# Kernel optimization log

Hardware: AMD Instinct MI355X
Metric: run time of the kernel (lower is better)

The kernel has to match this reference:

```python
import jax, jax.numpy as jnp
import numpy as np

C = 4096
IN_DIM = 256
OUT_DIM = 64
H = 4
NEG_SLOPE = 0.2


def setup_inputs() -> dict:
    key = jax.random.key(0)
    k_x, k_adj, k_w, k_as, k_ad = jax.random.split(key, 5)
    x = jax.random.normal(k_x, (C, IN_DIM), dtype=jnp.float32)
    adj = jax.random.randint(k_adj, (C, C), 0, 2, dtype=jnp.int32)
    # xavier_uniform for Linear(in, out*H): bound = sqrt(6/(fan_in+fan_out))
    bw = float(np.sqrt(6.0 / (IN_DIM + OUT_DIM * H)))
    W = jax.random.uniform(k_w, (IN_DIM, OUT_DIM * H), minval=-bw, maxval=bw, dtype=jnp.float32)
    ba = float(np.sqrt(6.0 / (H + OUT_DIM)))
    a_src = jax.random.uniform(k_as, (H, OUT_DIM), minval=-ba, maxval=ba, dtype=jnp.float32)
    a_dst = jax.random.uniform(k_ad, (H, OUT_DIM), minval=-ba, maxval=ba, dtype=jnp.float32)
    return {"x": x, "adj": adj, "W": W, "a_src": a_src, "a_dst": a_dst}


def reference(x, adj, W, a_src, a_dst):
    # h: [C, H, D] -> h_heads: [H, C, D]
    h = (x @ W).reshape(C, H, OUT_DIM)
    h_heads = jnp.transpose(h, (1, 0, 2))
    # per-node additive attention logits: [H, C]
    alpha_src = jnp.einsum('hcd,hd->hc', h_heads, a_src)
    alpha_dst = jnp.einsum('hcd,hd->hc', h_heads, a_dst)
    # broadcast scores e: [H, C, C]
    e = alpha_src[:, :, None] + alpha_dst[:, None, :]
    e = jnp.where(e >= 0, e, NEG_SLOPE * e)  # LeakyReLU
    e = jnp.where(adj[None, :, :] == 0, -jnp.inf, e)
    attn = jax.nn.softmax(e, axis=-1)  # [H, C, C]
    out = jnp.einsum('hcj,hjd->hcd', attn, h_heads)  # [H, C, D]
    return jnp.transpose(out, (1, 0, 2)).reshape(C, H * OUT_DIM)
```

## Files before the change

kernel.cpp:

```cpp
#include <hip/hip_runtime.h>
#include <math.h>

#define CN 4096
#define KDIM 256
#define ND 256
#define NH 4
#define DD 64
#define NEG 0.2f
#define L2E 1.44269504f

typedef __attribute__((ext_vector_type(8))) short short8;
typedef __attribute__((ext_vector_type(4))) float floatx4;

union S8I4 { int i[4]; short8 s; };

__device__ inline unsigned bfbits_rne(float f) {
  unsigned u = __float_as_uint(f);
  u += 0x7fffu + ((u >> 16) & 1u);
  return u >> 16;
}
__device__ inline float bf2f(unsigned hi) { return __uint_as_float(hi << 16); }

__device__ inline int pack2_trunc(float a, float b) {
  return (int)__builtin_amdgcn_perm(__float_as_uint(b), __float_as_uint(a), 0x07060302u);
}

#define GLDS(gp, lp, sz)                                                        \
  __builtin_amdgcn_global_load_lds(                                             \
      (const __attribute__((address_space(1))) void*)(gp),                      \
      (__attribute__((address_space(3))) void*)(lp), (sz), 0, 0)

__global__ __launch_bounds__(256) void k_prep(const int* __restrict__ adj,
                                              unsigned long long* __restrict__ mbits,
                                              const float* __restrict__ W,
                                              unsigned short* __restrict__ WT_hi,
                                              unsigned short* __restrict__ WT_lo) {
  const int bx = blockIdx.x;
  const int t = threadIdx.x;
  if (bx < 4096) {
    const int w = t >> 6, lane = t & 63;
    const size_t base = ((size_t)(bx * 4 + w)) * 1024;
#pragma unroll 4
    for (int it = 0; it < 16; ++it) {
      const size_t idx = base + (size_t)it * 64 + lane;
      const unsigned long long m = __ballot(adj[idx] != 0);
      if (lane == 0) mbits[idx >> 6] = m;
    }
  } else {
    const int c = (bx - 4096) * 4 + (t >> 6);
    const int k0 = (t & 63) * 4;
    unsigned h[4], l[4];
#pragma unroll
    for (int j = 0; j < 4; ++j) {
      const float w = W[(size_t)(k0 + j) * ND + c];
      h[j] = bfbits_rne(w);
      l[j] = bfbits_rne(w - bf2f(h[j]));
    }
    uint2 vh, vl;
    vh.x = h[0] | (h[1] << 16); vh.y = h[2] | (h[3] << 16);
    vl.x = l[0] | (l[1] << 16); vl.y = l[2] | (l[3] << 16);
    *(uint2*)&WT_hi[(size_t)c * KDIM + k0] = vh;
    *(uint2*)&WT_lo[(size_t)c * KDIM + k0] = vl;
  }
}

__global__ __launch_bounds__(256, 2) void k_gemm_h(const float* __restrict__ x,
                                                   const unsigned short* __restrict__ WT_hi,
                                                   const unsigned short* __restrict__ WT_lo,
                                                   const float* __restrict__ a_src,
                                                   const float* __restrict__ a_dst,
                                                   unsigned short* __restrict__ hT,
                                                   float* __restrict__ asrc,
                                                   float* __restrict__ adst) {
  __shared__ __align__(16) unsigned short Whi_s[64 * 264];
  __shared__ __align__(16) unsigned short Wlo_s[64 * 264];
  const int t = threadIdx.x;
  const int lane = t & 63, ww = t >> 6;
  const int n = lane & 15, q = lane >> 4;
  const int head = blockIdx.x;
  const int i0 = blockIdx.y * 64 + ww * 16;
#pragma unroll
  for (int p = 0; p < 8; ++p) {
    const int s = p * 256 + t;
    const int c = s >> 5, kseg = s & 31;
    const size_t g = (size_t)(head * 64 + c) * KDIM + kseg * 8;
    *(short8*)&Whi_s[c * 264 + kseg * 8] = *(const short8*)(WT_hi + g);
    *(short8*)&Wlo_s[c * 264 + kseg * 8] = *(const short8*)(WT_lo + g);
  }
  const float* xr = x + (size_t)(i0 + n) * KDIM + q * 8;
  float4 xa = *(const float4*)(xr);
  float4 xb = *(const float4*)(xr + 4);
  __syncthreads();
  floatx4 acc[4] = {};
  for (int k0 = 0; k0 < KDIM; k0 += 32) {
    const float xs[8] = {xa.x, xa.y, xa.z, xa.w, xb.x, xb.y, xb.z, xb.w};
    if (k0 + 32 < KDIM) {
      xa = *(const float4*)(xr + k0 + 32);
      xb = *(const float4*)(xr + k0 + 36);
    }
    S8I4 Ah, Al;
#pragma unroll
    for (int e = 0; e < 4; ++e) {
      const unsigned h0 = bfbits_rne(xs[2 * e]), h1 = bfbits_rne(xs[2 * e + 1]);
      const float r0 = xs[2 * e] - bf2f(h0), r1 = xs[2 * e + 1] - bf2f(h1);
      Ah.i[e] = (int)(h0 | (h1 << 16));
      Al.i[e] = (int)(bfbits_rne(r0) | (bfbits_rne(r1) << 16));
    }
#pragma unroll
    for (int tt = 0; tt < 4; ++tt) {
      const int boff = (tt * 16 + n) * 264 + k0 + q * 8;
      const short8 Bh = *(const short8*)&Whi_s[boff];
      const short8 Bl = *(const short8*)&Wlo_s[boff];
      acc[tt] = __builtin_amdgcn_mfma_f32_16x16x32_bf16(Ah.s, Bh, acc[tt], 0, 0, 0);
      acc[tt] = __builtin_amdgcn_mfma_f32_16x16x32_bf16(Al.s, Bh, acc[tt], 0, 0, 0);
      acc[tt] = __builtin_amdgcn_mfma_f32_16x16x32_bf16(Ah.s, Bl, acc[tt], 0, 0, 0);
    }
  }
  unsigned short* hTb = hT + (size_t)head * DD * CN;
#pragma unroll
  for (int tt = 0; tt < 4; ++tt)
#pragma unroll
    for (int r = 0; r < 4; r += 2) {
      const unsigned d = bfbits_rne(acc[tt][r]) | (bfbits_rne(acc[tt][r + 1]) << 16);
      *(unsigned*)(hTb + (size_t)(tt * 16 + n) * CN + i0 + q * 4 + r) = d;
    }
  float ps[4] = {}, pd[4] = {};
#pragma unroll
  for (int tt = 0; tt < 4; ++tt) {
    const float as = a_src[head * DD + tt * 16 + n];
    const float ad = a_dst[head * DD + tt * 16 + n];
#pragma unroll
    for (int r = 0; r < 4; ++r) {
      ps[r] += acc[tt][r] * as;
      pd[r] += acc[tt][r] * ad;
    }
  }
#pragma unroll
  for (int off = 1; off < 16; off <<= 1)
#pragma unroll
    for (int r = 0; r < 4; ++r) {
      ps[r] += __shfl_xor(ps[r], off);
      pd[r] += __shfl_xor(pd[r], off);
    }
  if (n == 0) {
#pragma unroll
    for (int r = 0; r < 4; ++r) {
      asrc[head * CN + i0 + q * 4 + r] = ps[r] * L2E;
      adst[head * CN + i0 + q * 4 + r] = pd[r] * L2E;
    }
  }
}

__global__ __launch_bounds__(256, 2) void k_attn(const unsigned short* __restrict__ hT,
                                                 const unsigned* __restrict__ mbits32,
                                                 const float* __restrict__ asrc,
                                                 const float* __restrict__ adst,
                                                 float* __restrict__ out) {
  __shared__ __align__(16) char smem[4 * 2 * 8704];
  const int t = threadIdx.x;
  const int lane = t & 63, ww = t >> 6;
  const int n = lane & 15, q = lane >> 4;
  const int head = blockIdx.y;
  const int i0 = blockIdx.x * 32;
  const unsigned short* __restrict__ hTb = hT + (size_t)head * DD * CN;
  const float* __restrict__ adh = adst + head * CN;
  const int jbase = ww * 1024;

  float sp0 = asrc[head * CN + i0 + n];
  float sp1 = asrc[head * CN + i0 + 16 + n];
  asm volatile("" : "+v"(sp0), "+v"(sp1));

  const int dl = lane >> 3, jbl = (lane & 7) ^ (lane >> 3);
  const unsigned hoff = (unsigned)dl * CN + jbl * 8;
  const unsigned moff = (unsigned)(i0 + (lane >> 1)) * 128 + (lane & 1);
  char* const wbase = smem + ww * 2 * 8704;

  short8 ONES;
#pragma unroll
  for (int u = 0; u < 8; ++u) ONES[u] = (short)0x3F80;

  floatx4 acc[2][4] = {};
  floatx4 accz[2] = {};

  auto ISSUE = [&](int b, int j0) {
    char* base = wbase + b * 8704;
#pragma unroll
    for (int w8 = 0; w8 < 8; ++w8)
      GLDS(hTb + (size_t)(w8 * 8) * CN + hoff + j0, base + w8 * 1024, 16);
    GLDS(mbits32 + moff + (j0 >> 5), base + 8192, 4);
    GLDS(adh + j0 + lane, base + 8448, 4);
  };

  ISSUE(0, jbase);
  for (int c = 0; c < 16; ++c) {
    const int b = c & 1;
    const int jn = jbase + ((c + 1) & 15) * 64;
    ISSUE(b ^ 1, jn);
    asm volatile("s_waitcnt vmcnt(10)" ::: "memory");
    const char* base = wbase + b * 8704;
    short8 B[4][2];
#pragma unroll
    for (int tt = 0; tt < 4; ++tt)
#pragma unroll
      for (int f = 0; f < 2; ++f)
        B[tt][f] = *(const short8*)(base + (tt * 16 + n) * 128 +
                                    ((((f << 2) | q) ^ (n & 7)) << 4));
    const uint2 mk0 = *(const uint2*)(base + 8192 + n * 8);
    const uint2 mk1 = *(const uint2*)(base + 8192 + (16 + n) * 8);
    const float* adl = (const float*)(base + 8448);
#pragma unroll
    for (int f = 0; f < 2; ++f) {
      const float4 a0 = *(const float4*)(adl + f * 32 + q * 8);
      const float4 a1 = *(const float4*)(adl + f * 32 + q * 8 + 4);
      const float ade[8] = {a0.x, a0.y, a0.z, a0.w, a1.x, a1.y, a1.z, a1.w};
#pragma unroll
      for (int rg = 0; rg < 2; ++rg) {
        const unsigned mw = f ? (rg ? mk1.y : mk0.y) : (rg ? mk1.x : mk0.x);
        const unsigned mbyte = (mw >> (q * 8)) & 255u;
        const float sp = rg ? sp1 : sp0;
        float fv[8];
#pragma unroll
        for (int e = 0; e < 8; ++e) {
          float xv = sp + ade[e];
          xv = fmaxf(xv, NEG * xv);
          xv = ((mbyte >> e) & 1u) ? xv : -1e38f;
          fv[e] = __builtin_amdgcn_exp2f(xv);
        }
        S8I4 A;
#pragma unroll
        for (int e = 0; e < 4; ++e) A.i[e] = pack2_trunc(fv[2 * e], fv[2 * e + 1]);
        accz[rg] = __builtin_amdgcn_mfma_f32_16x16x32_bf16(A.s, ONES, accz[rg], 0, 0, 0);
#pragma unroll
        for (int tt = 0; tt < 4; ++tt)
          acc[rg][tt] =
              __builtin_amdgcn_mfma_f32_16x16x32_bf16(A.s, B[tt][f], acc[rg][tt], 0, 0, 0);
      }
    }
  }

  __syncthreads();
  float* red = (float*)smem;
  if (ww > 0) {
#pragma unroll
    for (int rg = 0; rg < 2; ++rg) {
      float* rb = red + ((ww - 1) * 2 + rg) * 1280;
#pragma unroll
      for (int tt = 0; tt < 4; ++tt)
#pragma unroll
        for (int r = 0; r < 4; ++r) rb[(tt * 4 + r) * 64 + lane] = acc[rg][tt][r];
#pragma unroll
      for (int r = 0; r < 4; ++r) rb[(16 + r) * 64 + lane] = accz[rg][r];
    }
  }
  __syncthreads();
  if (ww == 0) {
#pragma unroll
    for (int s = 0; s < 3; ++s)
#pragma unroll
      for (int rg = 0; rg < 2; ++rg) {
        const float* rb = red + (s * 2 + rg) * 1280;
#pragma unroll
        for (int tt = 0; tt < 4; ++tt)
#pragma unroll
          for (int r = 0; r < 4; ++r) acc[rg][tt][r] += rb[(tt * 4 + r) * 64 + lane];
#pragma unroll
        for (int r = 0; r < 4; ++r) accz[rg][r] += rb[(16 + r) * 64 + lane];
      }
#pragma unroll
    for (int rg = 0; rg < 2; ++rg)
#pragma unroll
      for (int r = 0; r < 4; ++r) {
        const float iz = 1.0f / accz[rg][r];
        float* orow = out + (size_t)(i0 + rg * 16 + q * 4 + r) * ND + head * DD + n;
#pragma unroll
        for (int tt = 0; tt < 4; ++tt) orow[tt * 16] = acc[rg][tt][r] * iz;
      }
  }
}

extern "C" void kernel_launch(void* const* d_in, const int* in_sizes, int n_in,
                              void* d_out, int out_size, void* d_ws, size_t ws_size,
                              hipStream_t stream) {
  const float* x = (const float*)d_in[0];
  const int* adj = (const int*)d_in[1];
  const float* W = (const float*)d_in[2];
  const float* a_src = (const float*)d_in[3];
  const float* a_dst = (const float*)d_in[4];
  float* out = (float*)d_out;

  unsigned short* hT = (unsigned short*)d_ws;
  float* asrc = (float*)(hT + (size_t)NH * DD * CN);
  float* adst = asrc + (size_t)NH * CN;
  unsigned short* WT_hi = (unsigned short*)(adst + (size_t)NH * CN);
  unsigned short* WT_lo = WT_hi + (size_t)ND * KDIM;
  unsigned long long* mbits = (unsigned long long*)(WT_lo + (size_t)ND * KDIM);

  k_prep<<<dim3(4096 + ND / 4), 256, 0, stream>>>(adj, mbits, W, WT_hi, WT_lo);
  k_gemm_h<<<dim3(NH, CN / 64), 256, 0, stream>>>(x, WT_hi, WT_lo, a_src, a_dst,
                                                  hT, asrc, adst);
  k_attn<<<dim3(CN / 32, NH), 256, 0, stream>>>(hT, (const unsigned*)mbits,
                                                asrc, adst, out);
}
```

Baseline: 151.9 us.

## Split attention key range across eight waves with smaller per-wave chunks

```diff
diff --git a/kernel.cpp b/kernel.cpp
--- a/kernel.cpp
+++ b/kernel.cpp
@@ -151,12 +151,12 @@
   }
 }
 
-__global__ __launch_bounds__(256, 2) void k_attn(const unsigned short* __restrict__ hT,
+__global__ __launch_bounds__(512, 4) void k_attn(const unsigned short* __restrict__ hT,
                                                  const unsigned* __restrict__ mbits32,
                                                  const float* __restrict__ asrc,
                                                  const float* __restrict__ adst,
                                                  float* __restrict__ out) {
-  __shared__ __align__(16) char smem[4 * 2 * 8704];
+  __shared__ __align__(16) char smem[8 * 2 * 4608];
   const int t = threadIdx.x;
   const int lane = t & 63, ww = t >> 6;
   const int n = lane & 15, q = lane >> 4;
@@ -164,16 +164,16 @@
   const int i0 = blockIdx.x * 32;
   const unsigned short* __restrict__ hTb = hT + (size_t)head * DD * CN;
   const float* __restrict__ adh = adst + head * CN;
-  const int jbase = ww * 1024;
-
-  float sp0 = asrc[head * CN + i0 + n];
-  float sp1 = asrc[head * CN + i0 + 16 + n];
-  asm volatile("" : "+v"(sp0), "+v"(sp1));
-
-  const int dl = lane >> 3, jbl = (lane & 7) ^ (lane >> 3);
-  const unsigned hoff = (unsigned)dl * CN + jbl * 8;
-  const unsigned moff = (unsigned)(i0 + (lane >> 1)) * 128 + (lane & 1);
-  char* const wbase = smem + ww * 2 * 8704;
+  const int jbase = ww * 512;
+
+  const float sp0 = asrc[head * CN + i0 + n];
+  const float sp1 = asrc[head * CN + i0 + 16 + n];
+
+  const unsigned hoff =
+      (unsigned)(lane >> 2) * CN + (((lane & 3) ^ ((lane >> 3) & 3)) * 8);
+  const unsigned mrow = (unsigned)(i0 + (lane & 31)) * 128;
+  const unsigned arow = (unsigned)(lane & 31);
+  char* const wbase = smem + ww * 2 * 4608;
 
   short8 ONES;
 #pragma unroll
@@ -183,89 +183,88 @@
   floatx4 accz[2] = {};
 
   auto ISSUE = [&](int b, int j0) {
-    char* base = wbase + b * 8704;
-#pragma unroll
-    for (int w8 = 0; w8 < 8; ++w8)
-      GLDS(hTb + (size_t)(w8 * 8) * CN + hoff + j0, base + w8 * 1024, 16);
-    GLDS(mbits32 + moff + (j0 >> 5), base + 8192, 4);
-    GLDS(adh + j0 + lane, base + 8448, 4);
+    char* base = wbase + b * 4608;
+#pragma unroll
+    for (int g = 0; g < 4; ++g)
+      GLDS(hTb + (size_t)(g * 16) * CN + hoff + j0, base + g * 1024, 16);
+    GLDS(mbits32 + mrow + (j0 >> 5), base + 4096, 4);
+    GLDS(adh + j0 + arow, base + 4352, 4);
   };
 
   ISSUE(0, jbase);
   for (int c = 0; c < 16; ++c) {
-    const int b = c & 1;
-    const int jn = jbase + ((c + 1) & 15) * 64;
-    ISSUE(b ^ 1, jn);
-    asm volatile("s_waitcnt vmcnt(10)" ::: "memory");
-    const char* base = wbase + b * 8704;
-    short8 B[4][2];
+    if (c < 15) {
+      ISSUE((c + 1) & 1, jbase + (c + 1) * 32);
+      asm volatile("s_waitcnt vmcnt(6)" ::: "memory");
+    } else {
+      asm volatile("s_waitcnt vmcnt(0)" ::: "memory");
+    }
+    const char* base = wbase + (c & 1) * 4608;
+    short8 B[4];
 #pragma unroll
     for (int tt = 0; tt < 4; ++tt)
-#pragma unroll
-      for (int f = 0; f < 2; ++f)
-        B[tt][f] = *(const short8*)(base + (tt * 16 + n) * 128 +
-                                    ((((f << 2) | q) ^ (n & 7)) << 4));
-    const uint2 mk0 = *(const uint2*)(base + 8192 + n * 8);
-    const uint2 mk1 = *(const uint2*)(base + 8192 + (16 + n) * 8);
-    const float* adl = (const float*)(base + 8448);
-#pragma unroll
-    for (int f = 0; f < 2; ++f) {
-      const float4 a0 = *(const float4*)(adl + f * 32 + q * 8);
-      const float4 a1 = *(const float4*)(adl + f * 32 + q * 8 + 4);
-      const float ade[8] = {a0.x, a0.y, a0.z, a0.w, a1.x, a1.y, a1.z, a1.w};
-#pragma unroll
-      for (int rg = 0; rg < 2; ++rg) {
-        const unsigned mw = f ? (rg ? mk1.y : mk0.y) : (rg ? mk1.x : mk0.x);
-        const unsigned mbyte = (mw >> (q * 8)) & 255u;
-        const float sp = rg ? sp1 : sp0;
-        float fv[8];
-#pragma unroll
-        for (int e = 0; e < 8; ++e) {
-          float xv = sp + ade[e];
-          xv = fmaxf(xv, NEG * xv);
-          xv = ((mbyte >> e) & 1u) ? xv : -1e38f;
-          fv[e] = __builtin_amdgcn_exp2f(xv);
-        }
-        S8I4 A;
-#pragma unroll
-        for (int e = 0; e < 4; ++e) A.i[e] = pack2_trunc(fv[2 * e], fv[2 * e + 1]);
-        accz[rg] = __builtin_amdgcn_mfma_f32_16x16x32_bf16(A.s, ONES, accz[rg], 0, 0, 0);
-#pragma unroll
-        for (int tt = 0; tt < 4; ++tt)
-          acc[rg][tt] =
-              __builtin_amdgcn_mfma_f32_16x16x32_bf16(A.s, B[tt][f], acc[rg][tt], 0, 0, 0);
+      B[tt] = *(const short8*)(base + (tt * 16 + n) * 64 +
+                               ((q ^ ((n >> 1) & 3)) << 4));
+    const unsigned m0 = *(const unsigned*)(base + 4096 + n * 4);
+    const unsigned m1 = *(const unsigned*)(base + 4096 + (16 + n) * 4);
+    const float* adl = (const float*)(base + 4352);
+    const float4 a0 = *(const float4*)(adl + q * 8);
+    const float4 a1 = *(const float4*)(adl + q * 8 + 4);
+    const float ade[8] = {a0.x, a0.y, a0.z, a0.w, a1.x, a1.y, a1.z, a1.w};
+#pragma unroll
+    for (int rg = 0; rg < 2; ++rg) {
+      const unsigned mbyte = ((rg ? m1 : m0) >> (q * 8)) & 255u;
+      const float sp = rg ? sp1 : sp0;
+      float fv[8];
+#pragma unroll
+      for (int e = 0; e < 8; ++e) {
+        float xv = sp + ade[e];
+        xv = fmaxf(xv, NEG * xv);
+        xv = ((mbyte >> e) & 1u) ? xv : -1e38f;
+        fv[e] = __builtin_amdgcn_exp2f(xv);
       }
+      S8I4 A;
+#pragma unroll
+      for (int e = 0; e < 4; ++e) A.i[e] = pack2_trunc(fv[2 * e], fv[2 * e + 1]);
+      accz[rg] = __builtin_amdgcn_mfma_f32_16x16x32_bf16(A.s, ONES, accz[rg], 0, 0, 0);
+#pragma unroll
+      for (int tt = 0; tt < 4; ++tt)
+        acc[rg][tt] =
+            __builtin_amdgcn_mfma_f32_16x16x32_bf16(A.s, B[tt], acc[rg][tt], 0, 0, 0);
     }
   }
 
   __syncthreads();
   float* red = (float*)smem;
   if (ww > 0) {
+    float* rb = red + (ww - 1) * 2560;
 #pragma unroll
     for (int rg = 0; rg < 2; ++rg) {
-      float* rb = red + ((ww - 1) * 2 + rg) * 1280;
 #pragma unroll
       for (int tt = 0; tt < 4; ++tt)
 #pragma unroll
-        for (int r = 0; r < 4; ++r) rb[(tt * 4 + r) * 64 + lane] = acc[rg][tt][r];
-#pragma unroll
-      for (int r = 0; r < 4; ++r) rb[(16 + r) * 64 + lane] = accz[rg][r];
+        for (int r = 0; r < 4; ++r)
+          rb[(rg * 20 + tt * 4 + r) * 64 + lane] = acc[rg][tt][r];
+#pragma unroll
+      for (int r = 0; r < 4; ++r) rb[(rg * 20 + 16 + r) * 64 + lane] = accz[rg][r];
     }
   }
   __syncthreads();
   if (ww == 0) {
 #pragma unroll
-    for (int s = 0; s < 3; ++s)
+    for (int s = 0; s < 7; ++s) {
+      const float* rb = red + s * 2560;
 #pragma unroll
       for (int rg = 0; rg < 2; ++rg) {
-        const float* rb = red + (s * 2 + rg) * 1280;
 #pragma unroll
         for (int tt = 0; tt < 4; ++tt)
 #pragma unroll
-          for (int r = 0; r < 4; ++r) acc[rg][tt][r] += rb[(tt * 4 + r) * 64 + lane];
-#pragma unroll
-        for (int r = 0; r < 4; ++r) accz[rg][r] += rb[(16 + r) * 64 + lane];
+          for (int r = 0; r < 4; ++r)
+            acc[rg][tt][r] += rb[(rg * 20 + tt * 4 + r) * 64 + lane];
+#pragma unroll
+        for (int r = 0; r < 4; ++r) accz[rg][r] += rb[(rg * 20 + 16 + r) * 64 + lane];
       }
+    }
 #pragma unroll
     for (int rg = 0; rg < 2; ++rg)
 #pragma unroll
@@ -298,6 +297,6 @@
   k_prep<<<dim3(4096 + ND / 4), 256, 0, stream>>>(adj, mbits, W, WT_hi, WT_lo);
   k_gemm_h<<<dim3(NH, CN / 64), 256, 0, stream>>>(x, WT_hi, WT_lo, a_src, a_dst,
                                                   hT, asrc, adst);
-  k_attn<<<dim3(CN / 32, NH), 256, 0, stream>>>(hT, (const unsigned*)mbits,
+  k_attn<<<dim3(CN / 32, NH), 512, 0, stream>>>(hT, (const unsigned*)mbits,
                                                 asrc, adst, out);
 }
```

Measured after the change: 154.7 us. About the same (+1.8%).
